# Performance work log

Hardware: AMD Instinct MI355X
Metric: run time of the kernel (lower is better)

The kernel has to match this reference:

```python
import jax, jax.numpy as jnp
import numpy as np

PRUNE_RATIO = 0.5
MIXUP_ALPHA = 0.05


def setup_inputs() -> dict:
    key = jax.random.key(0)
    k1, k2 = jax.random.split(key)
    seq = jax.random.normal(k1, (16, 4096, 1024), dtype=jnp.float32)
    attn_weights = jax.random.normal(k2, (16, 4096), dtype=jnp.float32)
    return {"seq": seq, "attn_weights": attn_weights}


def reference(seq, attn_weights):
    # Eval-mode forward (adversarial_mix only fires in training mode).
    B, N, D = seq.shape
    k = max(1, int(N * (1.0 - PRUNE_RATIO)))  # number of kept tokens
    _, top_idx = jax.lax.top_k(attn_weights, k)  # (B, k) int32
    # gather selected tokens: (B, k, D)
    selected = jnp.take_along_axis(seq, top_idx[:, :, None], axis=1)
    # mask of pruned (non-selected) tokens: ones scattered to zero at top_idx
    batch_ids = jnp.arange(B)[:, None]
    mask = jnp.ones((B, N), dtype=seq.dtype).at[batch_ids, top_idx].set(0.0)
    # masked mean of pruned tokens, scaled by mixup_alpha -> one extra token
    rem_sum = jnp.einsum('bn,bnd->bd', mask, seq)              # (B, D)
    rem_cnt = jnp.sum(mask, axis=1, keepdims=True) + 1e-10     # (B, 1)
    rem_tok = (MIXUP_ALPHA * rem_sum / rem_cnt)[:, None, :]    # (B, 1, D)
    return jnp.concatenate([selected, rem_tok], axis=1)         # (B, k+1, D)
```

## Files before the change

kernel.cpp:

```cpp
#include <hip/hip_runtime.h>

#define BATCH 16
#define NTOK  4096
#define DIM   1024
#define KSEL  2048
#define NPRUNE 2048

#define NBIN 4096
#define RTHREADS 1024
#define RBLK 4
#define TPT (NTOK / RTHREADS)
#define BPT (NBIN / RTHREADS)

#define GROWS 32
#define GBLK (NTOK / GROWS)

typedef __attribute__((ext_vector_type(4))) float f32x4;

__global__ __launch_bounds__(1024) void rank_kernel(
    const float* __restrict__ w, int* __restrict__ rk) {
  __shared__ unsigned int s_cnt[NBIN];
  __shared__ unsigned int s_base[NBIN];
  __shared__ unsigned int s_cur[NBIN];
  __shared__ unsigned long long s_key[NTOK];
  __shared__ unsigned int s_wsum[16];
  __shared__ unsigned int s_woff[16];

  const int b = blockIdx.y;
  const int qq = blockIdx.x;
  const int t = threadIdx.x;
  const float* wb = w + (size_t)b * NTOK;

  for (int i = t; i < NBIN; i += RTHREADS) s_cnt[i] = 0;
  __syncthreads();

  unsigned int inv[TPT];
  unsigned int bin[TPT];
#pragma unroll
  for (int p = 0; p < TPT; ++p) {
    const int j = p * RTHREADS + t;
    const unsigned int u = __float_as_uint(wb[j]);
    const unsigned int s = (u & 0x80000000u) ? ~u : (u | 0x80000000u);
    const unsigned int iv = ~s;
    inv[p] = iv; bin[p] = iv >> 20;
    atomicAdd(&s_cnt[bin[p]], 1u);
  }
  __syncthreads();

  unsigned int c[BPT];
  unsigned int lsum = 0;
#pragma unroll
  for (int i = 0; i < BPT; ++i) { c[i] = s_cnt[t * BPT + i]; lsum += c[i]; }
  const int lane = t & 63, wid = t >> 6;
  unsigned int v = lsum;
  for (int d = 1; d < 64; d <<= 1) {
    unsigned int up = __shfl_up(v, d, 64);
    if (lane >= d) v += up;
  }
  if (lane == 63) s_wsum[wid] = v;
  __syncthreads();
  if (t == 0) {
    unsigned int run = 0;
    for (int i = 0; i < 16; ++i) { const unsigned int x = s_wsum[i]; s_woff[i] = run; run += x; }
  }
  __syncthreads();
  unsigned int excl = v - lsum + s_woff[wid];
#pragma unroll
  for (int i = 0; i < BPT; ++i) {
    s_base[t * BPT + i] = excl;
    s_cur[t * BPT + i] = excl;
    excl += c[i];
  }
  __syncthreads();

#pragma unroll
  for (int p = 0; p < TPT; ++p) {
    const int j = p * RTHREADS + t;
    const unsigned long long key =
        ((unsigned long long)inv[p] << 32) | (unsigned int)j;
    const unsigned int pos = atomicAdd(&s_cur[bin[p]], 1u);
    s_key[pos] = key;
  }
  __syncthreads();

  const int tok = qq * RTHREADS + t;
  const unsigned int u = __float_as_uint(wb[tok]);
  const unsigned int s = (u & 0x80000000u) ? ~u : (u | 0x80000000u);
  const unsigned int iv = ~s;
  const unsigned long long key =
      ((unsigned long long)iv << 32) | (unsigned int)tok;
  const unsigned int bb = iv >> 20;
  const unsigned int st = s_base[bb];
  const unsigned int en = s_cur[bb];
  unsigned int r = st;
  for (unsigned int q = st; q < en; ++q) r += (s_key[q] < key);
  rk[b * NTOK + tok] = (int)r;
}

__global__ __launch_bounds__(256) void gather_kernel(
    const float* __restrict__ seq, const int* __restrict__ rk,
    float* __restrict__ out, float* __restrict__ part) {
  const int b = blockIdx.y, g = blockIdx.x;
  const int lane = threadIdx.x;
  const f32x4* src = (const f32x4*)(seq + (size_t)b * NTOK * DIM) +
                     (size_t)g * GROWS * (DIM / 4);
  const int* rkb = rk + b * NTOK + g * GROWS;
  f32x4* outb = (f32x4*)(out + (size_t)b * (KSEL + 1) * DIM);
  f32x4 acc = {0.f, 0.f, 0.f, 0.f};
#pragma unroll 8
  for (int i = 0; i < GROWS; ++i) {
    const f32x4 x = __builtin_nontemporal_load(src + (size_t)i * (DIM / 4) + lane);
    const int r = rkb[i];
    if (r < KSEL) {
      __builtin_nontemporal_store(x, outb + (size_t)r * (DIM / 4) + lane);
    } else {
      acc += x;
    }
  }
  f32x4* pdst = (f32x4*)(part + ((size_t)b * GBLK + g) * DIM);
  pdst[lane] = acc;
}

__global__ __launch_bounds__(256) void reduce_kernel(
    const float* __restrict__ part, float* __restrict__ out, float scale) {
  __shared__ f32x4 s_acc[4][64];
  const int b = blockIdx.y, qq = blockIdx.x;
  const int t = threadIdx.x, g = t >> 6, col = t & 63;
  const int c4 = qq * 64 + col;
  const f32x4* p = (const f32x4*)(part + (size_t)b * GBLK * DIM);
  f32x4 acc = {0.f, 0.f, 0.f, 0.f};
#pragma unroll
  for (int i = 0; i < GBLK / 4; ++i) {
    const int ch = g + 4 * i;
    acc += p[(size_t)ch * (DIM / 4) + c4];
  }
  s_acc[g][col] = acc;
  __syncthreads();
  if (g == 0) {
    f32x4 r = (s_acc[0][col] + s_acc[1][col]) + (s_acc[2][col] + s_acc[3][col]);
    r *= scale;
    f32x4* dst = (f32x4*)(out + (size_t)b * (KSEL + 1) * DIM +
                          (size_t)KSEL * DIM);
    dst[c4] = r;
  }
}

extern "C" void kernel_launch(void* const* d_in, const int* in_sizes, int n_in,
                              void* d_out, int out_size, void* d_ws, size_t ws_size,
                              hipStream_t stream) {
  (void)in_sizes; (void)n_in; (void)out_size; (void)ws_size;
  const float* seq = (const float*)d_in[0];
  const float* w   = (const float*)d_in[1];
  float* out = (float*)d_out;

  int* rk = (int*)d_ws;
  float* part = (float*)(rk + BATCH * NTOK);

  rank_kernel<<<dim3(RBLK, BATCH), RTHREADS, 0, stream>>>(w, rk);
  gather_kernel<<<dim3(GBLK, BATCH), 256, 0, stream>>>(seq, rk, out, part);
  const float scale = (float)(0.05 / (2048.0 + 1e-10));
  reduce_kernel<<<dim3(4, BATCH), 256, 0, stream>>>(part, out, scale);
}
```

Measured before the change: 404.9 us.

## Fuse brute-force rank computation into gather kernel, drop histogram rank kernel

Removes the separate histogram/bucket-sort rank kernel, which ran on only 64 blocks, along with its global rank buffer. Each gather block now loads all 4096 attention weights for its batch into LDS as order-preserving 64-bit keys. It then computes the ranks of its 32 rows by brute-force comparison, with 8 threads per row, each scanning a rotated span to spread LDS bank accesses. This trades redundant per-block compute and 32KB of LDS, which may limit occupancy, for one fewer launch and rank work that overlaps with the memory-bound gather.

New measurement: 412.1 us. Within noise of the previous version (+1.8%).

```diff
diff --git a/kernel.cpp b/kernel.cpp
--- a/kernel.cpp
+++ b/kernel.cpp
@@ -6,111 +6,64 @@
 #define KSEL  2048
 #define NPRUNE 2048
 
-#define NBIN 4096
-#define RTHREADS 1024
-#define RBLK 4
-#define TPT (NTOK / RTHREADS)
-#define BPT (NBIN / RTHREADS)
-
 #define GROWS 32
 #define GBLK (NTOK / GROWS)
+#define PARTS 8
+#define SPAN (NTOK / PARTS)
 
 typedef __attribute__((ext_vector_type(4))) float f32x4;
 
-__global__ __launch_bounds__(1024) void rank_kernel(
-    const float* __restrict__ w, int* __restrict__ rk) {
-  __shared__ unsigned int s_cnt[NBIN];
-  __shared__ unsigned int s_base[NBIN];
-  __shared__ unsigned int s_cur[NBIN];
+__global__ __launch_bounds__(256) void gather_rank_kernel(
+    const float* __restrict__ seq, const float* __restrict__ w,
+    float* __restrict__ out, float* __restrict__ part) {
   __shared__ unsigned long long s_key[NTOK];
-  __shared__ unsigned int s_wsum[16];
-  __shared__ unsigned int s_woff[16];
+  __shared__ int s_rank[GROWS];
 
-  const int b = blockIdx.y;
-  const int qq = blockIdx.x;
+  const int b = blockIdx.y, g = blockIdx.x;
   const int t = threadIdx.x;
   const float* wb = w + (size_t)b * NTOK;
 
-  for (int i = t; i < NBIN; i += RTHREADS) s_cnt[i] = 0;
-  __syncthreads();
-
-  unsigned int inv[TPT];
-  unsigned int bin[TPT];
+  const f32x4* w4 = (const f32x4*)wb;
 #pragma unroll
-  for (int p = 0; p < TPT; ++p) {
-    const int j = p * RTHREADS + t;
-    const unsigned int u = __float_as_uint(wb[j]);
-    const unsigned int s = (u & 0x80000000u) ? ~u : (u | 0x80000000u);
-    const unsigned int iv = ~s;
-    inv[p] = iv; bin[p] = iv >> 20;
-    atomicAdd(&s_cnt[bin[p]], 1u);
+  for (int k = 0; k < NTOK / (256 * 4); ++k) {
+    const int i4 = k * 256 + t;
+    const f32x4 x = w4[i4];
+#pragma unroll
+    for (int c = 0; c < 4; ++c) {
+      const int j = i4 * 4 + c;
+      const unsigned int u = __float_as_uint(x[c]);
+      const unsigned int s = (u & 0x80000000u) ? ~u : (u | 0x80000000u);
+      s_key[j] = ((unsigned long long)(~s) << 32) | (unsigned int)j;
+    }
   }
   __syncthreads();
 
-  unsigned int c[BPT];
-  unsigned int lsum = 0;
-#pragma unroll
-  for (int i = 0; i < BPT; ++i) { c[i] = s_cnt[t * BPT + i]; lsum += c[i]; }
-  const int lane = t & 63, wid = t >> 6;
-  unsigned int v = lsum;
-  for (int d = 1; d < 64; d <<= 1) {
-    unsigned int up = __shfl_up(v, d, 64);
-    if (lane >= d) v += up;
+  const int row = t >> 3;
+  const int p = t & 7;
+  const int tok = g * GROWS + row;
+  const unsigned long long ki = s_key[tok];
+  unsigned int cnt = 0;
+  const int base = p * SPAN;
+#pragma unroll 8
+  for (int k = 0; k < SPAN; ++k) {
+    const int j = base + ((k + 2 * p) & (SPAN - 1));
+    cnt += (s_key[j] < ki);
   }
-  if (lane == 63) s_wsum[wid] = v;
-  __syncthreads();
-  if (t == 0) {
-    unsigned int run = 0;
-    for (int i = 0; i < 16; ++i) { const unsigned int x = s_wsum[i]; s_woff[i] = run; run += x; }
-  }
-  __syncthreads();
-  unsigned int excl = v - lsum + s_woff[wid];
-#pragma unroll
-  for (int i = 0; i < BPT; ++i) {
-    s_base[t * BPT + i] = excl;
-    s_cur[t * BPT + i] = excl;
-    excl += c[i];
-  }
+  cnt += __shfl_down(cnt, 4, 8);
+  cnt += __shfl_down(cnt, 2, 8);
+  cnt += __shfl_down(cnt, 1, 8);
+  if (p == 0) s_rank[row] = (int)cnt;
   __syncthreads();
 
-#pragma unroll
-  for (int p = 0; p < TPT; ++p) {
-    const int j = p * RTHREADS + t;
-    const unsigned long long key =
-        ((unsigned long long)inv[p] << 32) | (unsigned int)j;
-    const unsigned int pos = atomicAdd(&s_cur[bin[p]], 1u);
-    s_key[pos] = key;
-  }
-  __syncthreads();
-
-  const int tok = qq * RTHREADS + t;
-  const unsigned int u = __float_as_uint(wb[tok]);
-  const unsigned int s = (u & 0x80000000u) ? ~u : (u | 0x80000000u);
-  const unsigned int iv = ~s;
-  const unsigned long long key =
-      ((unsigned long long)iv << 32) | (unsigned int)tok;
-  const unsigned int bb = iv >> 20;
-  const unsigned int st = s_base[bb];
-  const unsigned int en = s_cur[bb];
-  unsigned int r = st;
-  for (unsigned int q = st; q < en; ++q) r += (s_key[q] < key);
-  rk[b * NTOK + tok] = (int)r;
-}
-
-__global__ __launch_bounds__(256) void gather_kernel(
-    const float* __restrict__ seq, const int* __restrict__ rk,
-    float* __restrict__ out, float* __restrict__ part) {
-  const int b = blockIdx.y, g = blockIdx.x;
-  const int lane = threadIdx.x;
+  const int lane = t;
   const f32x4* src = (const f32x4*)(seq + (size_t)b * NTOK * DIM) +
                      (size_t)g * GROWS * (DIM / 4);
-  const int* rkb = rk + b * NTOK + g * GROWS;
   f32x4* outb = (f32x4*)(out + (size_t)b * (KSEL + 1) * DIM);
   f32x4 acc = {0.f, 0.f, 0.f, 0.f};
 #pragma unroll 8
   for (int i = 0; i < GROWS; ++i) {
     const f32x4 x = __builtin_nontemporal_load(src + (size_t)i * (DIM / 4) + lane);
-    const int r = rkb[i];
+    const int r = s_rank[i];
     if (r < KSEL) {
       __builtin_nontemporal_store(x, outb + (size_t)r * (DIM / 4) + lane);
     } else {
@@ -153,11 +106,9 @@
   const float* w   = (const float*)d_in[1];
   float* out = (float*)d_out;
 
-  int* rk = (int*)d_ws;
-  float* part = (float*)(rk + BATCH * NTOK);
+  float* part = (float*)d_ws;
 
-  rank_kernel<<<dim3(RBLK, BATCH), RTHREADS, 0, stream>>>(w, rk);
-  gather_kernel<<<dim3(GBLK, BATCH), 256, 0, stream>>>(seq, rk, out, part);
+  gather_rank_kernel<<<dim3(GBLK, BATCH), 256, 0, stream>>>(seq, w, out, part);
   const float scale = (float)(0.05 / (2048.0 + 1e-10));
   reduce_kernel<<<dim3(4, BATCH), 256, 0, stream>>>(part, out, scale);
 }
```
